# Kernel optimization log

Measured on AMD Instinct MI355X. Metric: run time of the kernel, lower is better.

## Reference

```python
import jax, jax.numpy as jnp
import numpy as np

PATCH = 4   # patch_size
TOPK = 2    # top_k

B, H, W, C = 4, 128, 128, 256
FF, E = 1024, 4


def setup_inputs() -> dict:
    key = jax.random.key(0)
    k1, k2, k3, k4 = jax.random.split(key, 4)
    x = jax.random.normal(k1, (B, H, W, C), dtype=jnp.float32)
    Wg = jax.random.normal(k2, (E, C), dtype=jnp.float32) * 0.01   # router gate (std=0.01 init)
    lim1 = (6.0 / (C + FF)) ** 0.5                                  # xavier_uniform bounds
    W1 = jax.random.uniform(k3, (E, FF, C), minval=-lim1, maxval=lim1, dtype=jnp.float32)
    b1 = jnp.zeros((E, FF), dtype=jnp.float32)
    W2 = jax.random.uniform(k4, (E, C, FF), minval=-lim1, maxval=lim1, dtype=jnp.float32)
    b2 = jnp.zeros((E, C), dtype=jnp.float32)
    return {"x": x, "Wg": Wg, "W1": W1, "b1": b1, "W2": W2, "b2": b2}


def reference(x, Wg, W1, b1, W2, b2):
    Bs, Hs, Ws, Cs = x.shape
    Es = Wg.shape[0]
    ph = pw = PATCH
    nh, nw = Hs // ph, Ws // pw
    P = nh * nw
    # [B, nh, ph, nw, pw, C]
    xp = x.reshape(Bs, nh, ph, nw, pw, Cs)
    # --- router: per-patch avg pool + linear gate ---
    means = xp.mean(axis=(2, 4))                                  # [B, nh, nw, C]
    logits = jnp.einsum('bhwc,ec->bhwe', means, Wg).reshape(Bs, P, Es)
    probs = jax.nn.softmax(logits, axis=-1)
    w, idx = jax.lax.top_k(probs, TOPK)                           # [B, P, K]
    w = w / (w.sum(axis=-1, keepdims=True) + 1e-9)
    # dense combine weights per expert: [B, P, E]
    comb = (jax.nn.one_hot(idx, Es, dtype=w.dtype) * w[..., None]).sum(axis=-2)
    # --- expert dispatch/combine over patch tokens ---
    tokens = xp.transpose(0, 1, 3, 2, 4, 5).reshape(Bs, P, ph * pw, Cs)  # [B,P,T,C]
    out = jnp.zeros_like(tokens)
    for e in range(Es):  # small fixed expert set
        h = jax.nn.gelu(jnp.einsum('bptc,fc->bptf', tokens, W1[e]) + b1[e],
                        approximate=False)
        y = jnp.einsum('bptf,cf->bptc', h, W2[e]) + b2[e]
        out = out + comb[:, :, e, None, None] * y
    # reassemble patches -> [B, H, W, C]
    out = out.reshape(Bs, nh, nw, ph, pw, Cs).transpose(0, 1, 3, 2, 4, 5)
    return out.reshape(Bs, Hs, Ws, Cs)
```

## Files before the change

### kernel.cpp

```cpp
#include <hip/hip_runtime.h>
#include <hip/hip_bf16.h>
#include <cstdint>

#define NB 4
#define NH 128
#define NW 128
#define NC 256
#define NFF 1024
#define NE 4
#define NPATCH 4096
#define NPAIR 16
#define PPB 4
#define BM 64
#define FFC 256

typedef __attribute__((ext_vector_type(8))) short short8;
typedef __attribute__((ext_vector_type(8))) unsigned short ushort8;
typedef __attribute__((ext_vector_type(4))) float f32x4;

__device__ __forceinline__ unsigned short f2b(float f) {
  union { float f; uint32_t u; } v; v.f = f;
  uint32_t u = v.u + 0x7FFFu + ((v.u >> 16) & 1u);
  return (unsigned short)(u >> 16);
}

__device__ __forceinline__ float gelu_f(float v) {
  float u = v * v;
  float t = __builtin_fmaf(u, 0.044715f, 1.0f) * v;
  float e = __builtin_amdgcn_exp2f(t * -2.3022083f);
  return v * __builtin_amdgcn_rcpf(1.0f + e);
}

__device__ __forceinline__ void bar_lgkm() {
  asm volatile("s_waitcnt lgkmcnt(0)" ::: "memory");
  __builtin_amdgcn_s_barrier();
}

__global__ __launch_bounds__(256) void convert_kernel(
    const float* __restrict__ W1, const float* __restrict__ W2,
    unsigned short* __restrict__ W1b, unsigned short* __restrict__ W2b,
    int* __restrict__ cnt, int n) {
  int i = blockIdx.x * blockDim.x + threadIdx.x;
  if (i < NPAIR) cnt[i] = 0;
  if (i < n) {
    W1b[i] = f2b(W1[i]);
    W2b[i] = f2b(W2[i]);
  }
}

__global__ __launch_bounds__(256) void router_kernel(
    const float* __restrict__ x, const float* __restrict__ Wg,
    int* __restrict__ cnt, int* __restrict__ plist, float2* __restrict__ wlist) {
  int p = blockIdx.x;
  int b = p >> 10, pi = p & 1023;
  int phi = pi >> 5, pwi = pi & 31;
  int c = threadIdx.x;

  const float* base = x + (((size_t)(b * NH + phi * 4) * NW) + pwi * 4) * NC + c;
  float s = 0.f;
#pragma unroll
  for (int i = 0; i < 4; i++)
#pragma unroll
    for (int j = 0; j < 4; j++)
      s += base[(i * NW + j) * NC];
  float mean = s * (1.f / 16.f);

  __shared__ float m_lds[NC];
  __shared__ double logit_lds[NE];
  m_lds[c] = mean;
  __syncthreads();

  int wid = c >> 6, lane = c & 63;
  {
    const float* wg = Wg + wid * NC;
    double acc = 0.0;
#pragma unroll
    for (int q = 0; q < 4; q++)
      acc += (double)m_lds[lane + q * 64] * (double)wg[lane + q * 64];
    for (int off = 32; off; off >>= 1) acc += __shfl_down(acc, off);
    if (lane == 0) logit_lds[wid] = acc;
  }
  __syncthreads();

  if (c == 0) {
    double l[NE], pp[NE];
    double mx = -1e300;
#pragma unroll
    for (int i = 0; i < NE; i++) { l[i] = logit_lds[i]; mx = fmax(mx, l[i]); }
    double sum = 0.0;
#pragma unroll
    for (int i = 0; i < NE; i++) { pp[i] = exp(l[i] - mx); sum += pp[i]; }
#pragma unroll
    for (int i = 0; i < NE; i++) pp[i] /= sum;
    int i1 = 0; double p1 = pp[0];
    for (int i = 1; i < NE; i++) if (pp[i] > p1) { p1 = pp[i]; i1 = i; }
    int i2 = -1; double p2 = -1.0;
    for (int i = 0; i < NE; i++) {
      if (i == i1) continue;
      if (pp[i] > p2) { p2 = pp[i]; i2 = i; }
    }
    double den = p1 + p2 + 1e-9;
    float w1 = (float)(p1 / den), w2 = (float)(p2 / den);
    int pr = i1 * NE + i2;
    int pos = atomicAdd(&cnt[pr], 1);
    plist[pr * NPATCH + pos] = p;
    wlist[pr * NPATCH + pos] = make_float2(w1, w2);
  }
}

__global__ __launch_bounds__(64) void worklist_kernel(
    const int* __restrict__ cnt, int* __restrict__ wl) {
  int lane = threadIdx.x;
  if (lane < NPAIR) {
    int base = 0, mynb = 0;
    for (int q = 0; q < NPAIR; ++q) {
      int nb = (cnt[q] + PPB - 1) / PPB;
      if (q < lane) base += nb;
      if (q == lane) mynb = nb;
    }
    for (int i = 0; i < mynb; ++i)
      wl[1 + base + i] = (lane << 12) | (i * PPB);
    if (lane == NPAIR - 1) wl[0] = base + mynb;
  }
}

__global__ __launch_bounds__(512, 2) void ffn_kernel(
    const float* __restrict__ x, const float* __restrict__ b1,
    const float* __restrict__ b2, const unsigned short* __restrict__ W1b,
    const unsigned short* __restrict__ W2b, const int* __restrict__ cnt,
    const int* __restrict__ plist, const float2* __restrict__ wlist,
    const int* __restrict__ wl, float* __restrict__ out) {
  __shared__ unsigned short Xl[BM * NC];
  __shared__ unsigned short Hl[2][BM * FFC];

  int bid = blockIdx.x;
  if (bid >= wl[0]) return;
  int ent = wl[1 + bid];
  int pr = ent >> 12, pbase = ent & 4095;
  int e1 = pr >> 2, e2 = pr & 3;
  int n = cnt[pr];

  int tid = threadIdx.x, lane = tid & 63, wid = tid >> 6;
  int l15 = lane & 15;
  int kgrp = (lane >> 4) * 8;

  const int*    pl  = plist + pr * NPATCH + pbase;
  const float2* wlp = wlist + pr * NPATCH + pbase;

  float wvA[PPB], wvB[PPB];
#pragma unroll
  for (int q = 0; q < PPB; q++) {
    if (pbase + q < n) { float2 w = wlp[q]; wvA[q] = w.x; wvB[q] = w.y; }
    else { wvA[q] = 0.f; wvB[q] = 0.f; }
  }

  {
    int r  = tid >> 3;
    int c0 = (tid & 7) * 32;
    int pid = (pbase + (r >> 4) < n) ? pl[r >> 4] : -1;
    int t = r & 15;
    if (pid >= 0) {
      int b = pid >> 10, pi = pid & 1023;
      int phi = pi >> 5, pwi = pi & 31;
      const float* src =
          x + (((size_t)(b * NH + phi * 4 + (t >> 2)) * NW) + pwi * 4 + (t & 3)) * NC + c0;
#pragma unroll
      for (int q = 0; q < 4; q++) {
        float4 v0 = *reinterpret_cast<const float4*>(src + q * 8);
        float4 v1 = *reinterpret_cast<const float4*>(src + q * 8 + 4);
        ushort8 h;
        h[0] = f2b(v0.x); h[1] = f2b(v0.y); h[2] = f2b(v0.z); h[3] = f2b(v0.w);
        h[4] = f2b(v1.x); h[5] = f2b(v1.y); h[6] = f2b(v1.z); h[7] = f2b(v1.w);
        int boff = (r * 512 + (c0 + q * 8) * 2) ^ ((r & 7) << 4);
        *reinterpret_cast<ushort8*>((char*)Xl + boff) = h;
      }
    } else {
      ushort8 h = (ushort8)0;
#pragma unroll
      for (int q = 0; q < 4; q++) {
        int boff = (r * 512 + (c0 + q * 8) * 2) ^ ((r & 7) << 4);
        *reinterpret_cast<ushort8*>((char*)Xl + boff) = h;
      }
    }
  }
  bar_lgkm();

  if (wid < 4) {
    int wf = wid;
    const unsigned short* W1A = W1b + (size_t)e1 * NFF * NC;
    const unsigned short* W1B = W1b + (size_t)e2 * NFF * NC;
    const float* b1A = b1 + e1 * NFF;
    const float* b1B = b1 + e2 * NFF;

    f32x4 acc1[4][4];
    ushort4 hreg[16];

#pragma unroll 1
    for (int j = 0; j < 8; ++j) {
      const unsigned short* W1e = (j < 4) ? W1A : W1B;
      const float* b1e = (j < 4) ? b1A : b1B;
      int fc = j & 3;
#pragma unroll
      for (int a = 0; a < 4; a++)
#pragma unroll
        for (int b = 0; b < 4; b++)
#pragma unroll
          for (int q = 0; q < 4; q++) acc1[a][b][q] = 0.f;

#pragma unroll
      for (int ks = 0; ks < 8; ++ks) {
        int k = ks * 32 + kgrp;
        short8 bX[4];
#pragma unroll
        for (int nt = 0; nt < 4; nt++) {
          int row = nt * 16 + l15;
          int boff = (row * 512 + k * 2) ^ ((row & 7) << 4);
          bX[nt] = *reinterpret_cast<const short8*>((const char*)Xl + boff);
        }
        short8 aW[4];
#pragma unroll
        for (int ftl = 0; ftl < 4; ftl++) {
          int f = fc * FFC + wf * 64 + ftl * 16 + l15;
          aW[ftl] = *reinterpret_cast<const short8*>(W1e + (size_t)f * NC + k);
        }
        __builtin_amdgcn_s_setprio(1);
#pragma unroll
        for (int ftl = 0; ftl < 4; ftl++)
#pragma unroll
          for (int nt = 0; nt < 4; nt++)
            acc1[ftl][nt] = __builtin_amdgcn_mfma_f32_16x16x32_bf16(
                aW[ftl], bX[nt], acc1[ftl][nt], 0, 0, 0);
        __builtin_amdgcn_s_setprio(0);
      }

#pragma unroll
      for (int ftl = 0; ftl < 4; ftl++) {
        int f0 = wf * 64 + ftl * 16 + (lane >> 4) * 4;
        float4 bv = *reinterpret_cast<const float4*>(b1e + fc * FFC + f0);
#pragma unroll
        for (int nt = 0; nt < 4; nt++) {
          float w = (j < 4) ? wvA[nt] : wvB[nt];
          ushort4 hp;
          hp.x = f2b(gelu_f(acc1[ftl][nt][0] + bv.x) * w);
          hp.y = f2b(gelu_f(acc1[ftl][nt][1] + bv.y) * w);
          hp.z = f2b(gelu_f(acc1[ftl][nt][2] + bv.z) * w);
          hp.w = f2b(gelu_f(acc1[ftl][nt][3] + bv.w) * w);
          hreg[ftl * 4 + nt] = hp;
        }
      }
      unsigned short* Hb = &Hl[j & 1][0];
#pragma unroll
      for (int g = 0; g < 16; ++g) {
        int ftl = g >> 2, nt = g & 3;
        int token = nt * 16 + l15;
        int f0 = wf * 64 + ftl * 16 + (lane >> 4) * 4;
        int boff = (token * 512 + f0 * 2) ^ ((token & 7) << 4);
        *reinterpret_cast<ushort4*>((char*)Hb + boff) = hreg[g];
      }
      bar_lgkm();
    }
  } else {
    int wc = wid - 4;
    const unsigned short* W2A = W2b + (size_t)e1 * NC * NFF;
    const unsigned short* W2B = W2b + (size_t)e2 * NC * NFF;

    f32x4 acc2[4][4];
#pragma unroll
    for (int a = 0; a < 4; a++)
#pragma unroll
      for (int b = 0; b < 4; b++)
#pragma unroll
        for (int q = 0; q < 4; q++) acc2[a][b][q] = 0.f;

    bar_lgkm();

#pragma unroll 1
    for (int j = 0; j < 8; ++j) {
      const unsigned short* W2e = (j < 4) ? W2A : W2B;
      int fcp = j & 3;
      const unsigned short* Hb = &Hl[j & 1][0];
#pragma unroll
      for (int ks = 0; ks < 8; ++ks) {
        int kf = ks * 32 + kgrp;
        short8 aH[4];
#pragma unroll
        for (int rt = 0; rt < 4; rt++) {
          int row = rt * 16 + l15;
          int boff = (row * 512 + kf * 2) ^ ((row & 7) << 4);
          aH[rt] = *reinterpret_cast<const short8*>((const char*)Hb + boff);
        }
        short8 bW[4];
#pragma unroll
        for (int ct = 0; ct < 4; ct++) {
          int c = wc * 64 + ct * 16 + l15;
          bW[ct] = *reinterpret_cast<const short8*>(
              W2e + (size_t)c * NFF + fcp * FFC + kf);
        }
        __builtin_amdgcn_s_setprio(1);
#pragma unroll
        for (int ct = 0; ct < 4; ct++)
#pragma unroll
          for (int rt = 0; rt < 4; rt++)
            acc2[ct][rt] = __builtin_amdgcn_mfma_f32_16x16x32_bf16(
                aH[rt], bW[ct], acc2[ct][rt], 0, 0, 0);
        __builtin_amdgcn_s_setprio(0);
      }
      if (j < 7) bar_lgkm();
    }

    float b2A4[4], b2B4[4];
#pragma unroll
    for (int ct = 0; ct < 4; ct++) {
      int c = wc * 64 + ct * 16 + l15;
      b2A4[ct] = b2[e1 * NC + c];
      b2B4[ct] = b2[e2 * NC + c];
    }
#pragma unroll
    for (int rt = 0; rt < 4; rt++) {
      if (pbase + rt >= n) continue;
      int pid = pl[rt];
      float wA = wvA[rt], wB = wvB[rt];
      int b = pid >> 10, pi = pid & 1023;
      int phi = pi >> 5, pwi = pi & 31;
#pragma unroll
      for (int i2 = 0; i2 < 4; i2++) {
        int t = (lane >> 4) * 4 + i2;
        float* dst =
            out + (((size_t)(b * NH + phi * 4 + (t >> 2)) * NW) + pwi * 4 + (t & 3)) * NC;
#pragma unroll
        for (int ct = 0; ct < 4; ct++) {
          int c = wc * 64 + ct * 16 + l15;
          dst[c] = acc2[ct][rt][i2] + wA * b2A4[ct] + wB * b2B4[ct];
        }
      }
    }
  }
}

extern "C" void kernel_launch(void* const* d_in, const int* in_sizes, int n_in,
                              void* d_out, int out_size, void* d_ws, size_t ws_size,
                              hipStream_t stream) {
  const float* x  = (const float*)d_in[0];
  const float* Wg = (const float*)d_in[1];
  const float* W1 = (const float*)d_in[2];
  const float* b1 = (const float*)d_in[3];
  const float* W2 = (const float*)d_in[4];
  const float* b2 = (const float*)d_in[5];
  float* out = (float*)d_out;

  char* ws = (char*)d_ws;
  unsigned short* W1b = (unsigned short*)ws;
  unsigned short* W2b = (unsigned short*)(ws + (size_t)2 * 1024 * 1024);
  int*    cnt   = (int*)(ws + (size_t)4 * 1024 * 1024);
  int*    plist = (int*)(ws + (size_t)4 * 1024 * 1024 + 256);
  float2* wlist = (float2*)(ws + (size_t)4 * 1024 * 1024 + 256 +
                            (size_t)NPAIR * NPATCH * sizeof(int));
  int*    wl    = (int*)(ws + (size_t)5 * 1024 * 1024);

  convert_kernel<<<dim3(4096), dim3(256), 0, stream>>>(W1, W2, W1b, W2b, cnt, NE * NFF * NC);
  router_kernel<<<dim3(NPATCH), dim3(256), 0, stream>>>(x, Wg, cnt, plist, wlist);
  worklist_kernel<<<dim3(1), dim3(64), 0, stream>>>(cnt, wl);

  ffn_kernel<<<dim3(1040), dim3(512), 0, stream>>>(
      x, b1, b2, W1b, W2b, cnt, plist, wlist, wl, out);
}
```

Baseline: 461.0 us.

## Halve FF chunk size for higher occupancy and interleave worklist by expert pair

Reduces the FF chunk from 256 to 128, which halves the H double buffer in shared memory and the per-wave accumulator registers, and raises launch bounds from 2 to 4 blocks per CU. The worklist is reorganised so each of 8 first-expert groups pairs expert (x, y) with (x+8) and interleaves slots across groups; empty slots are marked -1 and exit early. The intent is higher occupancy and better L2 locality of expert weights across concurrently running blocks. In exchange there are twice as many barriers per block, more grid slots (including wasted empty ones), and the 8208-block grid relies on mx never exceeding 1025.

```diff
diff --git a/kernel.cpp b/kernel.cpp
--- a/kernel.cpp
+++ b/kernel.cpp
@@ -12,7 +12,8 @@
 #define NPAIR 16
 #define PPB 4
 #define BM 64
-#define FFC 256
+#define FFC 128
+#define NCHUNK_TOT 16
 
 typedef __attribute__((ext_vector_type(8))) short short8;
 typedef __attribute__((ext_vector_type(8))) unsigned short ushort8;
@@ -111,20 +112,26 @@
 __global__ __launch_bounds__(64) void worklist_kernel(
     const int* __restrict__ cnt, int* __restrict__ wl) {
   int lane = threadIdx.x;
-  if (lane < NPAIR) {
-    int base = 0, mynb = 0;
-    for (int q = 0; q < NPAIR; ++q) {
-      int nb = (cnt[q] + PPB - 1) / PPB;
-      if (q < lane) base += nb;
-      if (q == lane) mynb = nb;
-    }
-    for (int i = 0; i < mynb; ++i)
-      wl[1 + base + i] = (lane << 12) | (i * PPB);
-    if (lane == NPAIR - 1) wl[0] = base + mynb;
-  }
-}
-
-__global__ __launch_bounds__(512, 2) void ffn_kernel(
+  int cA[8], cB[8], mx = 0;
+#pragma unroll
+  for (int xc = 0; xc < 8; ++xc) {
+    cA[xc] = (cnt[xc] + PPB - 1) / PPB;
+    cB[xc] = (cnt[xc + 8] + PPB - 1) / PPB;
+    int t = cA[xc] + cB[xc];
+    mx = (t > mx) ? t : mx;
+  }
+  if (lane == 0) wl[0] = 8 * mx;
+  int x = lane & 7, sub = lane >> 3;
+  int nA = cA[x], tot = cA[x] + cB[x];
+  for (int r = sub; r < mx; r += 8) {
+    int ent = -1;
+    if (r < nA) ent = (x << 12) | (r * PPB);
+    else if (r < tot) ent = ((x + 8) << 12) | ((r - nA) * PPB);
+    wl[1 + x + 8 * r] = ent;
+  }
+}
+
+__global__ __launch_bounds__(512, 4) void ffn_kernel(
     const float* __restrict__ x, const float* __restrict__ b1,
     const float* __restrict__ b2, const unsigned short* __restrict__ W1b,
     const unsigned short* __restrict__ W2b, const int* __restrict__ cnt,
@@ -133,9 +140,10 @@
   __shared__ unsigned short Xl[BM * NC];
   __shared__ unsigned short Hl[2][BM * FFC];
 
-  int bid = blockIdx.x;
-  if (bid >= wl[0]) return;
-  int ent = wl[1 + bid];
+  int slot = blockIdx.x;
+  if (slot >= wl[0]) return;
+  int ent = wl[1 + slot];
+  if (ent < 0) return;
   int pr = ent >> 12, pbase = ent & 4095;
   int e1 = pr >> 2, e2 = pr & 3;
   int n = cnt[pr];
@@ -192,16 +200,16 @@
     const float* b1A = b1 + e1 * NFF;
     const float* b1B = b1 + e2 * NFF;
 
-    f32x4 acc1[4][4];
-    ushort4 hreg[16];
+    f32x4 acc1[2][4];
+    ushort4 hreg[8];
 
 #pragma unroll 1
-    for (int j = 0; j < 8; ++j) {
-      const unsigned short* W1e = (j < 4) ? W1A : W1B;
-      const float* b1e = (j < 4) ? b1A : b1B;
-      int fc = j & 3;
-#pragma unroll
-      for (int a = 0; a < 4; a++)
+    for (int j = 0; j < NCHUNK_TOT; ++j) {
+      const unsigned short* W1e = (j < 8) ? W1A : W1B;
+      const float* b1e = (j < 8) ? b1A : b1B;
+      int fc = j & 7;
+#pragma unroll
+      for (int a = 0; a < 2; a++)
 #pragma unroll
         for (int b = 0; b < 4; b++)
 #pragma unroll
@@ -217,15 +225,15 @@
           int boff = (row * 512 + k * 2) ^ ((row & 7) << 4);
           bX[nt] = *reinterpret_cast<const short8*>((const char*)Xl + boff);
         }
-        short8 aW[4];
-#pragma unroll
-        for (int ftl = 0; ftl < 4; ftl++) {
-          int f = fc * FFC + wf * 64 + ftl * 16 + l15;
+        short8 aW[2];
+#pragma unroll
+        for (int ftl = 0; ftl < 2; ftl++) {
+          int f = fc * FFC + wf * 32 + ftl * 16 + l15;
           aW[ftl] = *reinterpret_cast<const short8*>(W1e + (size_t)f * NC + k);
         }
         __builtin_amdgcn_s_setprio(1);
 #pragma unroll
-        for (int ftl = 0; ftl < 4; ftl++)
+        for (int ftl = 0; ftl < 2; ftl++)
 #pragma unroll
           for (int nt = 0; nt < 4; nt++)
             acc1[ftl][nt] = __builtin_amdgcn_mfma_f32_16x16x32_bf16(
@@ -234,12 +242,12 @@
       }
 
 #pragma unroll
-      for (int ftl = 0; ftl < 4; ftl++) {
-        int f0 = wf * 64 + ftl * 16 + (lane >> 4) * 4;
+      for (int ftl = 0; ftl < 2; ftl++) {
+        int f0 = wf * 32 + ftl * 16 + (lane >> 4) * 4;
         float4 bv = *reinterpret_cast<const float4*>(b1e + fc * FFC + f0);
 #pragma unroll
         for (int nt = 0; nt < 4; nt++) {
-          float w = (j < 4) ? wvA[nt] : wvB[nt];
+          float w = (j < 8) ? wvA[nt] : wvB[nt];
           ushort4 hp;
           hp.x = f2b(gelu_f(acc1[ftl][nt][0] + bv.x) * w);
           hp.y = f2b(gelu_f(acc1[ftl][nt][1] + bv.y) * w);
@@ -250,11 +258,11 @@
       }
       unsigned short* Hb = &Hl[j & 1][0];
 #pragma unroll
-      for (int g = 0; g < 16; ++g) {
+      for (int g = 0; g < 8; ++g) {
         int ftl = g >> 2, nt = g & 3;
         int token = nt * 16 + l15;
-        int f0 = wf * 64 + ftl * 16 + (lane >> 4) * 4;
-        int boff = (token * 512 + f0 * 2) ^ ((token & 7) << 4);
+        int f0 = wf * 32 + ftl * 16 + (lane >> 4) * 4;
+        int boff = (token * 256 + f0 * 2) ^ ((token & 7) << 4);
         *reinterpret_cast<ushort4*>((char*)Hb + boff) = hreg[g];
       }
       bar_lgkm();
@@ -275,18 +283,18 @@
     bar_lgkm();
 
 #pragma unroll 1
-    for (int j = 0; j < 8; ++j) {
-      const unsigned short* W2e = (j < 4) ? W2A : W2B;
-      int fcp = j & 3;
+    for (int j = 0; j < NCHUNK_TOT; ++j) {
+      const unsigned short* W2e = (j < 8) ? W2A : W2B;
+      int fcp = j & 7;
       const unsigned short* Hb = &Hl[j & 1][0];
 #pragma unroll
-      for (int ks = 0; ks < 8; ++ks) {
+      for (int ks = 0; ks < 4; ++ks) {
         int kf = ks * 32 + kgrp;
         short8 aH[4];
 #pragma unroll
         for (int rt = 0; rt < 4; rt++) {
           int row = rt * 16 + l15;
-          int boff = (row * 512 + kf * 2) ^ ((row & 7) << 4);
+          int boff = (row * 256 + kf * 2) ^ ((row & 7) << 4);
           aH[rt] = *reinterpret_cast<const short8*>((const char*)Hb + boff);
         }
         short8 bW[4];
@@ -305,7 +313,7 @@
                 aH[rt], bW[ct], acc2[ct][rt], 0, 0, 0);
         __builtin_amdgcn_s_setprio(0);
       }
-      if (j < 7) bar_lgkm();
+      if (j < NCHUNK_TOT - 1) bar_lgkm();
     }
 
     float b2A4[4], b2B4[4];
@@ -361,6 +369,6 @@
   router_kernel<<<dim3(NPATCH), dim3(256), 0, stream>>>(x, Wg, cnt, plist, wlist);
   worklist_kernel<<<dim3(1), dim3(64), 0, stream>>>(cnt, wl);
 
-  ffn_kernel<<<dim3(1040), dim3(512), 0, stream>>>(
+  ffn_kernel<<<dim3(8208), dim3(512), 0, stream>>>(
       x, b1, b2, W1b, W2b, cnt, plist, wlist, wl, out);
 }
```

Measured after the change: 438.2 us. -4.9%, faster.
